# Kernel tuning notes

Measured on AMD Instinct MI355X. Metric: run time of the kernel, lower is better.

## Reference

```python
import jax, jax.numpy as jnp
import numpy as np

B, C, H, W = 32, 3, 512, 512

def setup_inputs() -> dict:
    key = jax.random.key(0)
    k1, k2 = jax.random.split(key)
    # pixel values in [0, 255], matching the byte-image assumption of the module
    prediction = jax.random.uniform(k1, (B, C, H, W), dtype=jnp.float32) * 255.0
    target = jax.random.uniform(k2, (B, C, H, W), dtype=jnp.float32) * 255.0
    return {"prediction": prediction, "target": target}

def _v_channel(x):
    # Faithful to: clamp(x*1, 0, 255).byte() -> cv2 RGB2HSV -> V channel.
    # For uint8 images, OpenCV's V channel is exactly max(R, G, B); the byte
    # cast truncates fractional parts, reproduced here with floor.
    q = jnp.floor(jnp.clip(x, 0.0, 255.0))  # [B,3,H,W] quantized to integers
    return jnp.max(q, axis=1)  # [B,H,W] value channel = max over RGB

def reference(prediction, target):
    v_pred = _v_channel(prediction)   # [B,H,W]
    v_tgt = _v_channel(target)        # [B,H,W]
    # torch.min/max over dim=1 of [B,H,W] reduces the height axis -> [B,W]
    dark_loss = jnp.mean((jnp.min(v_pred, axis=1) - jnp.min(v_tgt, axis=1)) ** 2)
    bright_loss = jnp.mean((jnp.max(v_pred, axis=1) - jnp.max(v_tgt, axis=1)) ** 2)
    return dark_loss + bright_loss
```

## Files before the change

kernel.cpp:

```cpp
#include <hip/hip_runtime.h>
#include <cfloat>

#define B  32
#define C  3
#define H  512
#define W  512
#define HW (H * W)
#define CHW (C * H * W)
#define W4 (W / 4)

__device__ __forceinline__ float vchan(float a, float b, float c) {
    float m = fmaxf(fmaxf(a, b), c);
    m = fminf(fmaxf(m, 0.0f), 255.0f);
    return floorf(m);
}

__global__ __launch_bounds__(128) void s1_minmax(
        const float* __restrict__ pred, const float* __restrict__ tgt,
        float* __restrict__ ws, int HC, int rows) {
    const int b     = blockIdx.x / HC;
    const int chunk = blockIdx.x - b * HC;
    const int w4    = threadIdx.x;

    const float4* P = reinterpret_cast<const float4*>(pred) + (size_t)b * (CHW / 4);
    const float4* T = reinterpret_cast<const float4*>(tgt)  + (size_t)b * (CHW / 4);

    float4 mnP = make_float4( FLT_MAX,  FLT_MAX,  FLT_MAX,  FLT_MAX);
    float4 mxP = make_float4(-FLT_MAX, -FLT_MAX, -FLT_MAX, -FLT_MAX);
    float4 mnT = mnP;
    float4 mxT = mxP;

    const int h0 = chunk * rows;
    #pragma unroll 4
    for (int h = h0; h < h0 + rows; ++h) {
        const int base = h * W4 + w4;
        float4 a = P[base];
        float4 g = P[base +     (HW / 4)];
        float4 c2 = P[base + 2 * (HW / 4)];
        float v0 = vchan(a.x, g.x, c2.x);
        float v1 = vchan(a.y, g.y, c2.y);
        float v2 = vchan(a.z, g.z, c2.z);
        float v3 = vchan(a.w, g.w, c2.w);
        mnP.x = fminf(mnP.x, v0); mxP.x = fmaxf(mxP.x, v0);
        mnP.y = fminf(mnP.y, v1); mxP.y = fmaxf(mxP.y, v1);
        mnP.z = fminf(mnP.z, v2); mxP.z = fmaxf(mxP.z, v2);
        mnP.w = fminf(mnP.w, v3); mxP.w = fmaxf(mxP.w, v3);
        a  = T[base];
        g  = T[base +     (HW / 4)];
        c2 = T[base + 2 * (HW / 4)];
        v0 = vchan(a.x, g.x, c2.x);
        v1 = vchan(a.y, g.y, c2.y);
        v2 = vchan(a.z, g.z, c2.z);
        v3 = vchan(a.w, g.w, c2.w);
        mnT.x = fminf(mnT.x, v0); mxT.x = fmaxf(mxT.x, v0);
        mnT.y = fminf(mnT.y, v1); mxT.y = fmaxf(mxT.y, v1);
        mnT.z = fminf(mnT.z, v2); mxT.z = fmaxf(mxT.z, v2);
        mnT.w = fminf(mnT.w, v3); mxT.w = fmaxf(mxT.w, v3);
    }

    const size_t arr = (size_t)B * HC * W4;
    const size_t o   = ((size_t)b * HC + chunk) * W4 + w4;
    float4* wsv = reinterpret_cast<float4*>(ws);
    wsv[o]           = mnP;
    wsv[o + arr]     = mxP;
    wsv[o + 2 * arr] = mnT;
    wsv[o + 3 * arr] = mxT;
}

__global__ __launch_bounds__(256) void s2a_reduce(
        const float* __restrict__ ws, double* __restrict__ partial, int HC) {
    const int i = blockIdx.x * 256 + threadIdx.x;
    const int b = i / W;
    const int w = i - b * W;

    const size_t arr = (size_t)B * HC * W;
    const float* minP = ws;
    const float* maxP = ws + arr;
    const float* minT = ws + 2 * arr;
    const float* maxT = ws + 3 * arr;

    float mnP = FLT_MAX, mxP = -FLT_MAX, mnT = FLT_MAX, mxT = -FLT_MAX;
    for (int c = 0; c < HC; ++c) {
        const size_t o = ((size_t)b * HC + c) * W + w;
        mnP = fminf(mnP, minP[o]);
        mxP = fmaxf(mxP, maxP[o]);
        mnT = fminf(mnT, minT[o]);
        mxT = fmaxf(mxT, maxT[o]);
    }
    const float dmin = mnP - mnT;
    const float dmax = mxP - mxT;
    double s = (double)dmin * (double)dmin + (double)dmax * (double)dmax;

    __shared__ double sd[256];
    sd[threadIdx.x] = s;
    __syncthreads();
    for (int st = 128; st > 0; st >>= 1) {
        if (threadIdx.x < st) sd[threadIdx.x] += sd[threadIdx.x + st];
        __syncthreads();
    }
    if (threadIdx.x == 0) partial[blockIdx.x] = sd[0];
}

__global__ __launch_bounds__(64) void s2b_final(
        const double* __restrict__ partial, float* __restrict__ out) {
    __shared__ double sd[64];
    sd[threadIdx.x] = partial[threadIdx.x];
    __syncthreads();
    for (int st = 32; st > 0; st >>= 1) {
        if (threadIdx.x < st) sd[threadIdx.x] += sd[threadIdx.x + st];
        __syncthreads();
    }
    if (threadIdx.x == 0) out[0] = (float)(sd[0] / (double)(B * W));
}

extern "C" void kernel_launch(void* const* d_in, const int* in_sizes, int n_in,
                              void* d_out, int out_size, void* d_ws, size_t ws_size,
                              hipStream_t stream) {
    const float* pred = (const float*)d_in[0];
    const float* tgt  = (const float*)d_in[1];
    float* out = (float*)d_out;
    float* wsf = (float*)d_ws;

    int HC = 16;
    while (HC > 1 &&
           (size_t)4 * B * HC * W * sizeof(float) + 64 * sizeof(double) > ws_size) {
        HC >>= 1;
    }
    const int rows = H / HC;

    hipLaunchKernelGGL(s1_minmax, dim3(B * HC), dim3(128), 0, stream,
                       pred, tgt, wsf, HC, rows);

    double* partial = (double*)(wsf + (size_t)4 * B * HC * W);
    hipLaunchKernelGGL(s2a_reduce, dim3(64), dim3(256), 0, stream,
                       wsf, partial, HC);
    hipLaunchKernelGGL(s2b_final, dim3(1), dim3(64), 0, stream,
                       partial, out);
}
```

Before: 46.10 us.

## Defer clamp/floor to reduction and split height across more blocks

After: 53.40 us. 15.8% more time.

```diff
diff --git a/kernel.cpp b/kernel.cpp
--- a/kernel.cpp
+++ b/kernel.cpp
@@ -9,10 +9,8 @@
 #define CHW (C * H * W)
 #define W4 (W / 4)
 
-__device__ __forceinline__ float vchan(float a, float b, float c) {
-    float m = fmaxf(fmaxf(a, b), c);
-    m = fminf(fmaxf(m, 0.0f), 255.0f);
-    return floorf(m);
+__device__ __forceinline__ float max3f(float a, float b, float c) {
+    return fmaxf(fmaxf(a, b), c);
 }
 
 __global__ __launch_bounds__(128) void s1_minmax(
@@ -34,13 +32,13 @@
     #pragma unroll 4
     for (int h = h0; h < h0 + rows; ++h) {
         const int base = h * W4 + w4;
-        float4 a = P[base];
-        float4 g = P[base +     (HW / 4)];
+        float4 a  = P[base];
+        float4 g  = P[base +     (HW / 4)];
         float4 c2 = P[base + 2 * (HW / 4)];
-        float v0 = vchan(a.x, g.x, c2.x);
-        float v1 = vchan(a.y, g.y, c2.y);
-        float v2 = vchan(a.z, g.z, c2.z);
-        float v3 = vchan(a.w, g.w, c2.w);
+        float v0 = max3f(a.x, g.x, c2.x);
+        float v1 = max3f(a.y, g.y, c2.y);
+        float v2 = max3f(a.z, g.z, c2.z);
+        float v3 = max3f(a.w, g.w, c2.w);
         mnP.x = fminf(mnP.x, v0); mxP.x = fmaxf(mxP.x, v0);
         mnP.y = fminf(mnP.y, v1); mxP.y = fmaxf(mxP.y, v1);
         mnP.z = fminf(mnP.z, v2); mxP.z = fmaxf(mxP.z, v2);
@@ -48,10 +46,10 @@
         a  = T[base];
         g  = T[base +     (HW / 4)];
         c2 = T[base + 2 * (HW / 4)];
-        v0 = vchan(a.x, g.x, c2.x);
-        v1 = vchan(a.y, g.y, c2.y);
-        v2 = vchan(a.z, g.z, c2.z);
-        v3 = vchan(a.w, g.w, c2.w);
+        v0 = max3f(a.x, g.x, c2.x);
+        v1 = max3f(a.y, g.y, c2.y);
+        v2 = max3f(a.z, g.z, c2.z);
+        v3 = max3f(a.w, g.w, c2.w);
         mnT.x = fminf(mnT.x, v0); mxT.x = fmaxf(mxT.x, v0);
         mnT.y = fminf(mnT.y, v1); mxT.y = fmaxf(mxT.y, v1);
         mnT.z = fminf(mnT.z, v2); mxT.z = fmaxf(mxT.z, v2);
@@ -67,11 +65,18 @@
     wsv[o + 3 * arr] = mxT;
 }
 
+__device__ __forceinline__ float qclip(float m) {
+    return floorf(fminf(fmaxf(m, 0.0f), 255.0f));
+}
+
 __global__ __launch_bounds__(256) void s2a_reduce(
         const float* __restrict__ ws, double* __restrict__ partial, int HC) {
-    const int i = blockIdx.x * 256 + threadIdx.x;
-    const int b = i / W;
-    const int w = i - b * W;
+    const int p  = threadIdx.x & 63;
+    const int q  = threadIdx.x >> 6;
+    const int i  = blockIdx.x * 64 + p;
+    const int b  = i / W;
+    const int w  = i - b * W;
+    const int QC = HC >> 2;
 
     const size_t arr = (size_t)B * HC * W;
     const float* minP = ws;
@@ -80,33 +85,44 @@
     const float* maxT = ws + 3 * arr;
 
     float mnP = FLT_MAX, mxP = -FLT_MAX, mnT = FLT_MAX, mxT = -FLT_MAX;
-    for (int c = 0; c < HC; ++c) {
+    const int c0 = q * QC;
+    for (int c = c0; c < c0 + QC; ++c) {
         const size_t o = ((size_t)b * HC + c) * W + w;
         mnP = fminf(mnP, minP[o]);
         mxP = fmaxf(mxP, maxP[o]);
         mnT = fminf(mnT, minT[o]);
         mxT = fmaxf(mxT, maxT[o]);
     }
-    const float dmin = mnP - mnT;
-    const float dmax = mxP - mxT;
-    double s = (double)dmin * (double)dmin + (double)dmax * (double)dmax;
 
-    __shared__ double sd[256];
-    sd[threadIdx.x] = s;
+    __shared__ float4 s4[256];
+    s4[threadIdx.x] = make_float4(mnP, mxP, mnT, mxT);
     __syncthreads();
-    for (int st = 128; st > 0; st >>= 1) {
+
+    __shared__ double sd[64];
+    if (q == 0) {
+        float4 v0 = s4[p], v1 = s4[p + 64], v2 = s4[p + 128], v3 = s4[p + 192];
+        float fmnP = fminf(fminf(v0.x, v1.x), fminf(v2.x, v3.x));
+        float fmxP = fmaxf(fmaxf(v0.y, v1.y), fmaxf(v2.y, v3.y));
+        float fmnT = fminf(fminf(v0.z, v1.z), fminf(v2.z, v3.z));
+        float fmxT = fmaxf(fmaxf(v0.w, v1.w), fmaxf(v2.w, v3.w));
+        const float dmin = qclip(fmnP) - qclip(fmnT);
+        const float dmax = qclip(fmxP) - qclip(fmxT);
+        sd[p] = (double)dmin * (double)dmin + (double)dmax * (double)dmax;
+    }
+    __syncthreads();
+    for (int st = 32; st > 0; st >>= 1) {
         if (threadIdx.x < st) sd[threadIdx.x] += sd[threadIdx.x + st];
         __syncthreads();
     }
     if (threadIdx.x == 0) partial[blockIdx.x] = sd[0];
 }
 
-__global__ __launch_bounds__(64) void s2b_final(
+__global__ __launch_bounds__(256) void s2b_final(
         const double* __restrict__ partial, float* __restrict__ out) {
-    __shared__ double sd[64];
+    __shared__ double sd[256];
     sd[threadIdx.x] = partial[threadIdx.x];
     __syncthreads();
-    for (int st = 32; st > 0; st >>= 1) {
+    for (int st = 128; st > 0; st >>= 1) {
         if (threadIdx.x < st) sd[threadIdx.x] += sd[threadIdx.x + st];
         __syncthreads();
     }
@@ -121,9 +137,9 @@
     float* out = (float*)d_out;
     float* wsf = (float*)d_ws;
 
-    int HC = 16;
-    while (HC > 1 &&
-           (size_t)4 * B * HC * W * sizeof(float) + 64 * sizeof(double) > ws_size) {
+    int HC = 128;
+    while (HC > 4 &&
+           (size_t)4 * B * HC * W * sizeof(float) + 256 * sizeof(double) > ws_size) {
         HC >>= 1;
     }
     const int rows = H / HC;
@@ -132,8 +148,8 @@
                        pred, tgt, wsf, HC, rows);
 
     double* partial = (double*)(wsf + (size_t)4 * B * HC * W);
-    hipLaunchKernelGGL(s2a_reduce, dim3(64), dim3(256), 0, stream,
+    hipLaunchKernelGGL(s2a_reduce, dim3(256), dim3(256), 0, stream,
                        wsf, partial, HC);
-    hipLaunchKernelGGL(s2b_final, dim3(1), dim3(64), 0, stream,
+    hipLaunchKernelGGL(s2b_final, dim3(1), dim3(256), 0, stream,
                        partial, out);
 }
```
